# Performance work log

Hardware: AMD Instinct MI355X
Metric: run time of the kernel (lower is better)

## Reference

```python
import jax, jax.numpy as jnp
import numpy as np

L = 12; D = 768; H = 12; HD = D // H
P = 16; IMG = 224; NPATCH = (IMG // P) ** 2
NCLS = 1000; B = 32
GAMMA = 0.01; MIN_TOKENS = 16; EPS = 1e-6
SCALE = HD ** -0.5


def _ln(x, w, b, eps=1e-6):
    mu = x.mean(-1, keepdims=True)
    var = ((x - mu) ** 2).mean(-1, keepdims=True)
    return (x - mu) * jax.lax.rsqrt(var + eps) * w + b


def setup_inputs() -> dict:
    key = jax.random.key(0)
    ks = jax.random.split(key, 16)
    s = 0.02
    rn = lambda k, shape: jax.random.normal(k, shape, jnp.float32) * s
    return {
        'x': jax.random.normal(ks[0], (B, 3, IMG, IMG), jnp.float32),
        'patch_w': rn(ks[1], (D, 3, P, P)),
        'patch_b': jnp.zeros((D,), jnp.float32),
        'cls_token': rn(ks[2], (1, 1, D)),
        'pos_embed': rn(ks[3], (1, NPATCH + 1, D)),
        'ln1_w': jnp.ones((L, D), jnp.float32), 'ln1_b': jnp.zeros((L, D), jnp.float32),
        'qkv_w': rn(ks[4], (L, D, 3 * D)), 'qkv_b': jnp.zeros((L, 3 * D), jnp.float32),
        'proj_w': rn(ks[5], (L, D, D)), 'proj_b': jnp.zeros((L, D), jnp.float32),
        'ln2_w': jnp.ones((L, D), jnp.float32), 'ln2_b': jnp.zeros((L, D), jnp.float32),
        'fc1_w': rn(ks[6], (L, D, 4 * D)), 'fc1_b': jnp.zeros((L, 4 * D), jnp.float32),
        'fc2_w': rn(ks[7], (L, 4 * D, D)), 'fc2_b': jnp.zeros((L, D), jnp.float32),
        'norm_w': jnp.ones((D,), jnp.float32), 'norm_b': jnp.zeros((D,), jnp.float32),
        'head_w': rn(ks[8], (D, NCLS)), 'head_b': jnp.zeros((NCLS,), jnp.float32),
    }


def _block(x, i, ln1_w, ln1_b, qkv_w, qkv_b, proj_w, proj_b, ln2_w, ln2_b, fc1_w, fc1_b, fc2_w, fc2_b):
    Bb, Ntok, _ = x.shape
    xn = _ln(x, ln1_w[i], ln1_b[i])
    qkv = (xn @ qkv_w[i] + qkv_b[i]).reshape(Bb, Ntok, 3, H, HD)
    qkv = qkv.transpose(2, 0, 3, 1, 4)  # [3, B, H, N, hd]
    q, k, v = qkv[0], qkv[1], qkv[2]
    # full N x N attention matrix, materialized as in the original module
    attn = jax.nn.softmax(jnp.einsum('bhqd,bhkd->bhqk', q, k) * SCALE, axis=-1)
    out = jnp.einsum('bhqk,bhkd->bhqd', attn, v)
    out = out.transpose(0, 2, 1, 3).reshape(Bb, Ntok, D) @ proj_w[i] + proj_b[i]
    x = x + out
    h = _ln(x, ln2_w[i], ln2_b[i])
    h = jax.nn.gelu(h @ fc1_w[i] + fc1_b[i], approximate=False)
    x = x + (h @ fc2_w[i] + fc2_b[i])
    return x, attn, v


def _importance(attn, v, eps):
    # Jacobian proxy: d(CLS)/d(patch_j) ~ attn[CLS->j] * ||v_j||
    v_norm = jnp.linalg.norm(v, axis=-1)            # [B, H, N]
    jac = attn[:, :, 0, 1:] * v_norm[:, :, 1:]       # [B, H, Npatch]
    importance = jac.mean(axis=(0, 1))               # batch-shared [Npatch]
    mass = importance.sum()
    rho = importance.std() / (importance.mean() + eps)
    return importance, mass, rho


def _keep_ratio(rho, mass, prev_mass, gamma, eps):
    drift = jnp.abs(mass - prev_mass) / (prev_mass + eps)
    return jnp.clip(1.0 - gamma * rho * (1.0 + drift), 0.0, 1.0)


def _select(importance, n_keep):
    _, idx = jax.lax.top_k(importance, n_keep)
    idx = jnp.sort(idx) + 1  # shift past CLS
    return jnp.concatenate([jnp.zeros((1,), idx.dtype), idx])  # always keep CLS


def reference(x, patch_w, patch_b, cls_token, pos_embed, ln1_w, ln1_b, qkv_w, qkv_b,
              proj_w, proj_b, ln2_w, ln2_b, fc1_w, fc1_b, fc2_w, fc2_b,
              norm_w, norm_b, head_w, head_b):
    Bb = x.shape[0]
    feat = jax.lax.conv_general_dilated(x, patch_w, (P, P), 'VALID',
                                        dimension_numbers=('NCHW', 'OIHW', 'NCHW'))
    feat = feat.reshape(Bb, D, NPATCH).transpose(0, 2, 1) + patch_b  # [B, 196, D]
    xx = jnp.concatenate([jnp.broadcast_to(cls_token, (Bb, 1, D)), feat], axis=1) + pos_embed
    N = NPATCH
    prev_mass = None
    for i in range(L):
        xx, attn, v = _block(xx, i, ln1_w, ln1_b, qkv_w, qkv_b, proj_w, proj_b,
                             ln2_w, ln2_b, fc1_w, fc1_b, fc2_w, fc2_b)
        if N <= MIN_TOKENS:
            prev_mass = None
            continue
        imp, mass, rho = _importance(attn, v, EPS)
        if prev_mass is not None:
            kr = float(_keep_ratio(rho, mass, prev_mass, GAMMA, EPS))
            n_next = max(MIN_TOKENS, int(N * kr))
        else:
            n_next = N
        if n_next < N:
            keep_idx = _select(imp, n_next)
            xx = jnp.take(xx, keep_idx, axis=1)
            N = n_next
        prev_mass = mass
    xx = _ln(xx, norm_w, norm_b)
    return xx[:, 0] @ head_w + head_b
```

## Files before the change

kernel.cpp:

```cpp
#include <hip/hip_runtime.h>
#include <math.h>

#define DEV_INLINE __device__ __forceinline__

constexpr int BB     = 32;
constexpr int DMODEL = 768;
constexpr int NHEAD  = 12;
constexpr int NPATCH = 196;
constexpr int NTOK   = 197;
constexpr int NLAYER = 12;
constexpr int NCLASS = 1000;
constexpr int MTOT   = BB * NTOK;
constexpr int MPAD   = 6400;

typedef __attribute__((ext_vector_type(4))) float f32x4;
typedef __attribute__((ext_vector_type(8))) short bf16x8;

DEV_INLINE void split2(float x, unsigned short& hi, unsigned short& lo) {
    unsigned u = __builtin_bit_cast(unsigned, x);
    unsigned r = (u + 0x7FFFu + ((u >> 16) & 1u)) >> 16;
    hi = (unsigned short)r;
    float fh = __builtin_bit_cast(float, r << 16);
    float l = x - fh;
    unsigned ul = __builtin_bit_cast(unsigned, l);
    lo = (unsigned short)((ul + 0x7FFFu + ((ul >> 16) & 1u)) >> 16);
}

DEV_INLINE unsigned split_pack(float x) {
    unsigned short h, l; split2(x, h, l);
    return (unsigned)h | ((unsigned)l << 16);
}

DEV_INLINE float bf2f(unsigned short s) {
    return __builtin_bit_cast(float, ((unsigned)s) << 16);
}

DEV_INLINE void gload16(const unsigned short* g, unsigned short* l) {
    __builtin_amdgcn_global_load_lds(
        (const __attribute__((address_space(1))) unsigned int*)g,
        (__attribute__((address_space(3))) unsigned int*)l, 16, 0, 0);
}

DEV_INLINE int aswz(int m, int k) {
    return (k & ~31) + ((((k >> 3) & 3) ^ ((m >> 1) & 3)) << 3) + (k & 7);
}

DEV_INLINE float block_reduce_sum(float v, float* sbuf) {
    #pragma unroll
    for (int off = 32; off > 0; off >>= 1) v += __shfl_down(v, off, 64);
    int lane = threadIdx.x & 63, w = threadIdx.x >> 6;
    __syncthreads();
    if (lane == 0) sbuf[w] = v;
    __syncthreads();
    return sbuf[0] + sbuf[1] + sbuf[2] + sbuf[3];
}

__global__ void state_init(int* nTokPtr, int* prevValidPtr) {
    *nTokPtr = NTOK;
    *prevValidPtr = 0;
}

__global__ __launch_bounds__(256)
void cls_init(const float* __restrict__ cls, const float* __restrict__ pos,
              float* __restrict__ tok) {
    int b = blockIdx.x;
    for (int i = threadIdx.x; i < DMODEL; i += 256)
        tok[(size_t)b * NTOK * DMODEL + i] = cls[i] + pos[i];
}

__global__ __launch_bounds__(256)
void wconv_patch(const float* __restrict__ src, unsigned short* __restrict__ hi,
                 unsigned short* __restrict__ lo) {
    int id = blockIdx.x * 256 + threadIdx.x;
    if (id >= 768 * 96) return;
    int n = id / 96, ch = id % 96;
    int k = ch * 8;
    float4 a = *(const float4*)(src + (size_t)n * 768 + k);
    float4 b = *(const float4*)(src + (size_t)n * 768 + k + 4);
    unsigned short h[8], l[8];
    split2(a.x,h[0],l[0]); split2(a.y,h[1],l[1]); split2(a.z,h[2],l[2]); split2(a.w,h[3],l[3]);
    split2(b.x,h[4],l[4]); split2(b.y,h[5],l[5]); split2(b.z,h[6],l[6]); split2(b.w,h[7],l[7]);
    int npanel = n >> 7, c = n & 127;
    int kbi = k >> 5, chunk = (k >> 3) & 3;
    size_t base = ((size_t)npanel * 24 + kbi) * 4096
                + c * 32 + ((chunk ^ ((c >> 1) & 3)) << 3);
    bf16x8 hv, lv;
    #pragma unroll
    for (int j = 0; j < 8; ++j) { hv[j] = (short)h[j]; lv[j] = (short)l[j]; }
    *(bf16x8*)(hi + base) = hv;
    *(bf16x8*)(lo + base) = lv;
}

constexpr size_t WOFF_QKV  = 0;
constexpr size_t WOFF_PROJ = (size_t)768 * 2304;
constexpr size_t WOFF_FC1  = WOFF_PROJ + (size_t)768 * 768;
constexpr size_t WOFF_FC2  = WOFF_FC1 + (size_t)768 * 3072;
constexpr size_t WTOTAL    = WOFF_FC2 + (size_t)3072 * 768;

__global__ __launch_bounds__(256)
void wconv_layer(const float* __restrict__ qkvw, const float* __restrict__ projw,
                 const float* __restrict__ fc1w, const float* __restrict__ fc2w,
                 unsigned short* __restrict__ hi, unsigned short* __restrict__ lo) {
    __shared__ float tile[32][33];
    int bid = blockIdx.x;
    const float* src; int Kd, Nd; size_t dofs;
    if (bid < 1728)      { src = qkvw;  Kd = 768;  Nd = 2304; dofs = WOFF_QKV; }
    else if (bid < 2304) { bid -= 1728; src = projw; Kd = 768;  Nd = 768;  dofs = WOFF_PROJ; }
    else if (bid < 4608) { bid -= 2304; src = fc1w;  Kd = 768;  Nd = 3072; dofs = WOFF_FC1; }
    else                 { bid -= 4608; src = fc2w;  Kd = 3072; Nd = 768;  dofs = WOFF_FC2; }
    const int nkb = Kd >> 5;
    int ntx = Nd / 32;
    int n0 = (bid % ntx) * 32, k0 = (bid / ntx) * 32;
    int tx = threadIdx.x & 31, ty = threadIdx.x >> 5;
    #pragma unroll
    for (int i = 0; i < 32; i += 8)
        tile[ty + i][tx] = src[(size_t)(k0 + ty + i) * Nd + n0 + tx];
    __syncthreads();
    int t = threadIdx.x;
    if (t < 128) {
        int nl = t >> 2, chunk = t & 3;
        unsigned short h[8], l[8];
        #pragma unroll
        for (int j = 0; j < 8; ++j) split2(tile[chunk * 8 + j][nl], h[j], l[j]);
        int n = n0 + nl, k = k0 + chunk * 8;
        int npanel = n >> 7, c = n & 127;
        int kbi = k >> 5;
        size_t base = dofs + ((size_t)npanel * nkb + kbi) * 4096
                    + c * 32 + ((chunk ^ ((c >> 1) & 3)) << 3);
        bf16x8 hv, lv;
        #pragma unroll
        for (int j = 0; j < 8; ++j) { hv[j] = (short)h[j]; lv[j] = (short)l[j]; }
        *(bf16x8*)(hi + base) = hv;
        *(bf16x8*)(lo + base) = lv;
    }
}

template<int ASRC, int EPI>
__global__ __launch_bounds__(256)
void mfma_gemm(const unsigned short* __restrict__ Ahp,
               const unsigned short* __restrict__ Alp,
               const float* __restrict__ Af,
               const unsigned short* __restrict__ Wht,
               const unsigned short* __restrict__ Wlt,
               const float* __restrict__ bias,
               const float* __restrict__ resid,
               void* __restrict__ C, void* __restrict__ C2,
               int ldc, int K, int Mtot, int gm, int gn,
               const int* __restrict__ nTokPtr) {
    const int nTok = (ASRC == 0) ? *nTokPtr : NTOK;
    int nb = gm * gn;
    int o = blockIdx.x;
    int qd = nb >> 3, r8 = nb & 7;
    int xcd = o & 7, wi = o >> 3;
    int fin = (xcd < r8 ? xcd * (qd + 1) : r8 * (qd + 1) + (xcd - r8) * qd) + wi;
    int bm = fin / gn, bn = fin - bm * gn;
    const int m0 = bm * 128, n0 = bn * 128;
    if (m0 >= Mtot) return;
    if (ASRC == 0) {
        int ts = m0 % NTOK;
        if (!(ts < nTok || ts + 128 > NTOK)) return;
    }
    __shared__ unsigned short LDSu[16384];
    unsigned short* AhL = LDSu;
    unsigned short* AlL = LDSu + 4096;
    unsigned short* BhL = LDSu + 8192;
    unsigned short* BlL = LDSu + 12288;
    const int tid = threadIdx.x;
    const int lane = tid & 63, wid = tid >> 6;
    const int wm = wid >> 1, wn = wid & 1;
    const int fr = lane & 15, fg = lane >> 4;

    f32x4 acc[4][4];
    #pragma unroll
    for (int i = 0; i < 4; ++i)
        #pragma unroll
        for (int j = 0; j < 4; ++j) acc[i][j] = (f32x4){0.f, 0.f, 0.f, 0.f};

    const int nkb = K >> 5;
    const int wbase = wid * 512;
    const int g8 = tid * 8;

    int arow = 0, acp = 0, axor = 0, aoff0 = 0, aoff1 = 0;
    bool aval = false; size_t abase = 0;
    if constexpr (ASRC == 1) {
        arow = tid >> 1;
        acp  = (tid & 1) * 2;
        int am = m0 + arow;
        aval = am < Mtot;
        int b = am / NPATCH, pp = am - b * NPATCH;
        int py = pp / 14, px = pp - py * 14;
        abase = (size_t)b * (3 * 224 * 224) + (size_t)(py * 16) * 224 + px * 16;
        axor = (arow >> 1) & 3;
        aoff0 = arow * 32 + ((acp ^ axor) << 3);
        aoff1 = arow * 32 + (((acp + 1) ^ axor) << 3);
    }
    size_t arow_g = 0;
    if constexpr (ASRC == 0)
        arow_g = (size_t)(m0 + (tid >> 2)) * K + (tid & 3) * 8;

    for (int kbi = 0; kbi < nkb; ++kbi) {
        {
            size_t tb = ((size_t)bn * nkb + kbi) * 4096 + g8;
            gload16(Wht + tb,        &BhL[wbase]);
            gload16(Wht + tb + 2048, &BhL[wbase + 2048]);
            gload16(Wlt + tb,        &BlL[wbase]);
            gload16(Wlt + tb + 2048, &BlL[wbase + 2048]);
        }
        if constexpr (ASRC == 0) {
            size_t ab = arow_g + (size_t)kbi * 32;
            gload16(Ahp + ab,                  &AhL[wbase]);
            gload16(Ahp + ab + (size_t)64 * K, &AhL[wbase + 2048]);
            gload16(Alp + ab,                  &AlL[wbase]);
            gload16(Alp + ab + (size_t)64 * K, &AlL[wbase + 2048]);
        } else {
            const int kb = kbi << 5;
            float f[16] = {0,0,0,0,0,0,0,0,0,0,0,0,0,0,0,0};
            if (aval) {
                int k = kb + acp * 8;
                size_t off = abase + (size_t)(k >> 8) * (224 * 224)
                           + (size_t)((k >> 4) & 15) * 224;
                *(float4*)&f[0]  = *(const float4*)(Af + off);
                *(float4*)&f[4]  = *(const float4*)(Af + off + 4);
                *(float4*)&f[8]  = *(const float4*)(Af + off + 8);
                *(float4*)&f[12] = *(const float4*)(Af + off + 12);
            }
            unsigned ph[8], pl[8];
            #pragma unroll
            for (int j = 0; j < 8; ++j) {
                unsigned short h0, l0, h1, l1;
                split2(f[2 * j], h0, l0); split2(f[2 * j + 1], h1, l1);
                ph[j] = (unsigned)h0 | ((unsigned)h1 << 16);
                pl[j] = (unsigned)l0 | ((unsigned)l1 << 16);
            }
            *(uint4*)&AhL[aoff0] = *(uint4*)&ph[0];
            *(uint4*)&AhL[aoff1] = *(uint4*)&ph[4];
            *(uint4*)&AlL[aoff0] = *(uint4*)&pl[0];
            *(uint4*)&AlL[aoff1] = *(uint4*)&pl[4];
        }
        __syncthreads();
        bf16x8 ah[4], al4[4], bh4[4], bl4[4];
        #pragma unroll
        for (int i = 0; i < 4; ++i) {
            int row = wm * 64 + i * 16 + fr;
            int aoff = row * 32 + ((fg ^ ((row >> 1) & 3)) << 3);
            ah[i]  = *(const bf16x8*)&AhL[aoff];
            al4[i] = *(const bf16x8*)&AlL[aoff];
            int col = wn * 64 + i * 16 + fr;
            int boff = col * 32 + ((fg ^ ((col >> 1) & 3)) << 3);
            bh4[i] = *(const bf16x8*)&BhL[boff];
            bl4[i] = *(const bf16x8*)&BlL[boff];
        }
        #pragma unroll
        for (int i = 0; i < 4; ++i)
            #pragma unroll
            for (int j = 0; j < 4; ++j) {
                acc[i][j] = __builtin_amdgcn_mfma_f32_16x16x32_bf16(ah[i],  bh4[j], acc[i][j], 0, 0, 0);
                acc[i][j] = __builtin_amdgcn_mfma_f32_16x16x32_bf16(ah[i],  bl4[j], acc[i][j], 0, 0, 0);
                acc[i][j] = __builtin_amdgcn_mfma_f32_16x16x32_bf16(al4[i], bh4[j], acc[i][j], 0, 0, 0);
            }
        __syncthreads();
    }
    if constexpr (EPI == 0 || EPI == 2) {
        unsigned pk[4][4][4];
        #pragma unroll
        for (int i = 0; i < 4; ++i)
            #pragma unroll
            for (int j = 0; j < 4; ++j)
                #pragma unroll
                for (int e = 0; e < 4; ++e) {
                    int n = n0 + wn * 64 + j * 16 + fr;
                    float v = acc[i][j][e] + bias[n];
                    if constexpr (EPI == 2)
                        v = 0.5f * v * (1.0f + erff(v * 0.70710678118654752f));
                    pk[i][j][e] = split_pack(v);
                }
        const int rr = tid >> 4, cc = tid & 15;
        #pragma unroll
        for (int plane = 0; plane < 2; ++plane) {
            __syncthreads();
            #pragma unroll
            for (int i = 0; i < 4; ++i)
                #pragma unroll
                for (int j = 0; j < 4; ++j)
                    #pragma unroll
                    for (int e = 0; e < 4; ++e) {
                        int r = wm * 64 + i * 16 + fg * 4 + e;
                        int c = wn * 64 + j * 16 + fr;
                        LDSu[r * 128 + c] = (unsigned short)
                            (plane ? (pk[i][j][e] >> 16) : (pk[i][j][e] & 0xffffu));
                    }
            __syncthreads();
            unsigned short* Cp = (unsigned short*)(plane ? C2 : C);
            #pragma unroll
            for (int p = 0; p < 8; ++p) {
                int r = p * 16 + rr;
                int m = m0 + r;
                if (m < Mtot && (m % NTOK) < nTok) {
                    size_t dst;
                    if constexpr (EPI == 0)
                        dst = (size_t)m * ldc + n0 + cc * 8;
                    else
                        dst = (size_t)m * ldc + n0 + (cc >> 2) * 32
                            + (((cc & 3) ^ ((m >> 1) & 3)) << 3);
                    *(bf16x8*)(Cp + dst) = *(const bf16x8*)&LDSu[r * 128 + cc * 8];
                }
            }
        }
    } else {
        #pragma unroll
        for (int i = 0; i < 4; ++i)
            #pragma unroll
            for (int j = 0; j < 4; ++j)
                #pragma unroll
                for (int e = 0; e < 4; ++e) {
                    int m = m0 + wm * 64 + i * 16 + fg * 4 + e;
                    int n = n0 + wn * 64 + j * 16 + fr;
                    if (m >= Mtot) continue;
                    if (ASRC == 0 && (m % NTOK) >= nTok) continue;
                    float v = acc[i][j][e] + bias[n];
                    if constexpr (EPI == 1) {
                        ((float*)C)[(size_t)m * ldc + n] = v + resid[(size_t)m * ldc + n];
                    } else {
                        int b = m / NPATCH, pp = m - b * NPATCH;
                        v += resid[(size_t)(1 + pp) * DMODEL + n];
                        ((float*)C)[((size_t)b * NTOK + 1 + pp) * DMODEL + n] = v;
                    }
                }
    }
}

__global__ __launch_bounds__(256)
void ln_tok(const float* __restrict__ X, unsigned short* __restrict__ Yh,
            unsigned short* __restrict__ Yl,
            const float* __restrict__ w, const float* __restrict__ b,
            const int* __restrict__ nTokPtr) {
    int m = blockIdx.x;
    if ((m % NTOK) >= *nTokPtr) return;
    __shared__ float sbuf[4];
    __shared__ float yb[768];
    const float* x = X + (size_t)m * DMODEL;
    int tid = threadIdx.x;
    float v[3];
    #pragma unroll
    for (int i = 0; i < 3; i++) v[i] = x[tid + i * 256];
    float mu = block_reduce_sum(v[0] + v[1] + v[2], sbuf) * (1.0f / 768.0f);
    float d2 = 0.f;
    #pragma unroll
    for (int i = 0; i < 3; i++) { float d = v[i] - mu; d2 = fmaf(d, d, d2); }
    float var = block_reduce_sum(d2, sbuf) * (1.0f / 768.0f);
    float rstd = rsqrtf(var + 1e-6f);
    #pragma unroll
    for (int i = 0; i < 3; i++) {
        int idx = tid + i * 256;
        yb[idx] = (v[i] - mu) * rstd * w[idx] + b[idx];
    }
    __syncthreads();
    if (tid < 96) {
        bf16x8 hv, lv;
        #pragma unroll
        for (int j = 0; j < 8; ++j) {
            unsigned short h, l; split2(yb[tid * 8 + j], h, l);
            hv[j] = (short)h; lv[j] = (short)l;
        }
        size_t dst = (size_t)m * 768 + (tid >> 2) * 32
                   + (((tid & 3) ^ ((m >> 1) & 3)) << 3);
        *(bf16x8*)(Yh + dst) = hv;
        *(bf16x8*)(Yl + dst) = lv;
    }
}

__global__ __launch_bounds__(256)
void ln_cls(const float* __restrict__ X, float* __restrict__ Y,
            const float* __restrict__ w, const float* __restrict__ b) {
    int bb = blockIdx.x;
    __shared__ float sbuf[4];
    const float* x = X + (size_t)bb * NTOK * DMODEL;
    int tid = threadIdx.x;
    float v[3];
    #pragma unroll
    for (int i = 0; i < 3; i++) v[i] = x[tid + i * 256];
    float mu = block_reduce_sum(v[0] + v[1] + v[2], sbuf) * (1.0f / 768.0f);
    float d2 = 0.f;
    #pragma unroll
    for (int i = 0; i < 3; i++) { float d = v[i] - mu; d2 = fmaf(d, d, d2); }
    float var = block_reduce_sum(d2, sbuf) * (1.0f / 768.0f);
    float rstd = rsqrtf(var + 1e-6f);
    #pragma unroll
    for (int i = 0; i < 3; i++) {
        int idx = tid + i * 256;
        Y[(size_t)bb * DMODEL + idx] = (v[i] - mu) * rstd * w[idx] + b[idx];
    }
}

__global__ __launch_bounds__(256)
void attn_v4(const unsigned short* __restrict__ qh_g,
             const unsigned short* __restrict__ ql_g,
             unsigned short* __restrict__ oh_g,
             unsigned short* __restrict__ ol_g,
             float* __restrict__ jacg, const int* __restrict__ nTokPtr) {
    const int nTok = *nTokPtr;
    const int bh = blockIdx.x;
    const int b = bh / NHEAD, h = bh % NHEAD;
    const int q0 = blockIdx.y * 32;
    if (q0 >= nTok) return;
    __shared__ unsigned short Kh[64 * 64], Kl[64 * 64];
    __shared__ unsigned short Vth[64 * 64], Vtl[64 * 64];
    __shared__ unsigned short Ph[32 * 64], Pl[32 * 64];
    __shared__ float Ss[32][68];
    __shared__ float mrow[32], lrow[32], frow[32];
    __shared__ float s0row[256], vnrow[256];
    __shared__ float vnpart[64][4];
    const int tid = threadIdx.x;
    const int lane = tid & 63, wv = tid >> 6;
    const int fr = lane & 15, fg = lane >> 4;
    const int qh = wv >> 1, xh = wv & 1;

    bf16x8 qah[2], qal[2];
    {
        int q = q0 + qh * 16 + fr;
        int qe = q < nTok ? q : nTok - 1;
        const unsigned short* qrh = qh_g + (size_t)(b * NTOK + qe) * 2304 + h * 64;
        const unsigned short* qrl = ql_g + (size_t)(b * NTOK + qe) * 2304 + h * 64;
        #pragma unroll
        for (int s = 0; s < 2; ++s) {
            qah[s] = *(const bf16x8*)(qrh + s * 32 + fg * 8);
            qal[s] = *(const bf16x8*)(qrl + s * 32 + fg * 8);
        }
    }
    if (tid < 32) { mrow[tid] = -INFINITY; lrow[tid] = 0.f; frow[tid] = 1.f; }
    f32x4 oacc[2] = {{0,0,0,0},{0,0,0,0}};
    const int njt = (nTok + 63) >> 6;
    const int sj = tid & 63, sdh = tid >> 6;

    for (int jt = 0; jt < njt; ++jt) {
        const int jb = jt * 64;
        __syncthreads();
        {
            int j = jb + sj;
            bf16x8 kh0, kh1, kl0, kl1, vh0, vh1, vl0, vl1;
            if (j < nTok) {
                size_t rp = (size_t)(b * NTOK + j) * 2304 + h * 64;
                kh0 = *(const bf16x8*)(qh_g + rp + 768 + sdh * 16);
                kh1 = *(const bf16x8*)(qh_g + rp + 768 + sdh * 16 + 8);
                kl0 = *(const bf16x8*)(ql_g + rp + 768 + sdh * 16);
                kl1 = *(const bf16x8*)(ql_g + rp + 768 + sdh * 16 + 8);
                vh0 = *(const bf16x8*)(qh_g + rp + 1536 + sdh * 16);
                vh1 = *(const bf16x8*)(qh_g + rp + 1536 + sdh * 16 + 8);
                vl0 = *(const bf16x8*)(ql_g + rp + 1536 + sdh * 16);
                vl1 = *(const bf16x8*)(ql_g + rp + 1536 + sdh * 16 + 8);
            } else {
                bf16x8 z = {0,0,0,0,0,0,0,0};
                kh0=kh1=kl0=kl1=vh0=vh1=vl0=vl1 = z;
            }
            int c0 = sdh * 2;
            int ko0 = sj * 64 + ((c0 ^ (sj & 7)) << 3);
            int ko1 = sj * 64 + (((c0 + 1) ^ (sj & 7)) << 3);
            *(bf16x8*)&Kh[ko0] = kh0; *(bf16x8*)&Kh[ko1] = kh1;
            *(bf16x8*)&Kl[ko0] = kl0; *(bf16x8*)&Kl[ko1] = kl1;
            float pn = 0.f;
            #pragma unroll
            for (int i = 0; i < 16; ++i) {
                unsigned short vh = (unsigned short)(i < 8 ? vh0[i] : vh1[i - 8]);
                unsigned short vl = (unsigned short)(i < 8 ? vl0[i] : vl1[i - 8]);
                int d = sdh * 16 + i;
                int si = d * 64 + (((sj >> 3) ^ (d & 7)) << 3) + (sj & 7);
                Vth[si] = vh; Vtl[si] = vl;
                if (q0 == 0) {
                    float vf = bf2f(vh) + bf2f(vl);
                    pn = fmaf(vf, vf, pn);
                }
            }
            if (q0 == 0) vnpart[sj][sdh] = pn;
        }
        __syncthreads();
        {
            f32x4 sacc[2] = {{0,0,0,0},{0,0,0,0}};
            #pragma unroll
            for (int s = 0; s < 2; ++s)
                #pragma unroll
                for (int t = 0; t < 2; ++t) {
                    int j = xh * 32 + t * 16 + fr;
                    int off = j * 64 + (((s * 4 + fg) ^ (j & 7)) << 3);
                    bf16x8 kbh = *(const bf16x8*)&Kh[off];
                    bf16x8 kbl = *(const bf16x8*)&Kl[off];
                    sacc[t] = __builtin_amdgcn_mfma_f32_16x16x32_bf16(qah[s], kbh, sacc[t], 0, 0, 0);
                    sacc[t] = __builtin_amdgcn_mfma_f32_16x16x32_bf16(qah[s], kbl, sacc[t], 0, 0, 0);
                    sacc[t] = __builtin_amdgcn_mfma_f32_16x16x32_bf16(qal[s], kbh, sacc[t], 0, 0, 0);
                }
            #pragma unroll
            for (int t = 0; t < 2; ++t)
                #pragma unroll
                for (int e = 0; e < 4; ++e) {
                    int q = q0 + qh * 16 + fg * 4 + e;
                    int j = jb + xh * 32 + t * 16 + fr;
                    Ss[qh * 16 + fg * 4 + e][xh * 32 + t * 16 + fr] =
                        (q < nTok && j < nTok) ? sacc[t][e] * 0.125f : -INFINITY;
                }
        }
        __syncthreads();
        {
            int q = tid >> 3, s = tid & 7;
            bool rowok = (q0 + q) < nTok;
            float4 va = *(const float4*)&Ss[q][s * 8];
            float4 vb = *(const float4*)&Ss[q][s * 8 + 4];
            if (q0 == 0 && q == 0) {
                *(float4*)&s0row[jb + s * 8] = va;
                *(float4*)&s0row[jb + s * 8 + 4] = vb;
            }
            float mx = fmaxf(fmaxf(fmaxf(va.x, va.y), fmaxf(va.z, va.w)),
                             fmaxf(fmaxf(vb.x, vb.y), fmaxf(vb.z, vb.w)));
            #pragma unroll
            for (int o = 1; o < 8; o <<= 1) mx = fmaxf(mx, __shfl_xor(mx, o));
            float mold = mrow[q];
            float mnew = fmaxf(mold, mx);
            float e[8];
            float sum = 0.f;
            if (rowok) {
                e[0] = expf(va.x - mnew); e[1] = expf(va.y - mnew);
                e[2] = expf(va.z - mnew); e[3] = expf(va.w - mnew);
                e[4] = expf(vb.x - mnew); e[5] = expf(vb.y - mnew);
                e[6] = expf(vb.z - mnew); e[7] = expf(vb.w - mnew);
                sum = ((e[0] + e[1]) + (e[2] + e[3])) + ((e[4] + e[5]) + (e[6] + e[7]));
            } else {
                #pragma unroll
                for (int i = 0; i < 8; ++i) e[i] = 0.f;
            }
            #pragma unroll
            for (int o = 1; o < 8; o <<= 1) sum += __shfl_xor(sum, o);
            bf16x8 ph, pl;
            #pragma unroll
            for (int i = 0; i < 8; ++i) {
                unsigned u = __builtin_bit_cast(unsigned, e[i]);
                ph[i] = (short)(u >> 16);
                float r = e[i] - __builtin_bit_cast(float, u & 0xffff0000u);
                pl[i] = (short)(__builtin_bit_cast(unsigned, r) >> 16);
            }
            int poff = q * 64 + ((s ^ (q & 7)) << 3);
            *(bf16x8*)&Ph[poff] = ph;
            *(bf16x8*)&Pl[poff] = pl;
            if (s == 0 && rowok) {
                float f = expf(mold - mnew);
                lrow[q] = lrow[q] * f + sum;
                mrow[q] = mnew;
                frow[q] = f;
            }
            if (q0 == 0 && tid < 64) {
                int jj = jb + tid;
                if (jj < nTok)
                    vnrow[jj] = sqrtf(vnpart[tid][0] + vnpart[tid][1]
                                    + vnpart[tid][2] + vnpart[tid][3]);
            }
        }
        __syncthreads();
        {
            float fe[4];
            #pragma unroll
            for (int e = 0; e < 4; ++e) fe[e] = frow[qh * 16 + fg * 4 + e];
            #pragma unroll
            for (int t = 0; t < 2; ++t)
                #pragma unroll
                for (int e = 0; e < 4; ++e) oacc[t][e] *= fe[e];
            #pragma unroll
            for (int s = 0; s < 2; ++s) {
                int pr = qh * 16 + fr;
                int poff = pr * 64 + (((s * 4 + fg) ^ (pr & 7)) << 3);
                bf16x8 pah = *(const bf16x8*)&Ph[poff];
                bf16x8 pal = *(const bf16x8*)&Pl[poff];
                #pragma unroll
                for (int t = 0; t < 2; ++t) {
                    int d = xh * 32 + t * 16 + fr;
                    int voff = d * 64 + (((s * 4 + fg) ^ (d & 7)) << 3);
                    bf16x8 vbh = *(const bf16x8*)&Vth[voff];
                    bf16x8 vbl = *(const bf16x8*)&Vtl[voff];
                    oacc[t] = __builtin_amdgcn_mfma_f32_16x16x32_bf16(pah, vbh, oacc[t], 0, 0, 0);
                    oacc[t] = __builtin_amdgcn_mfma_f32_16x16x32_bf16(pah, vbl, oacc[t], 0, 0, 0);
                    oacc[t] = __builtin_amdgcn_mfma_f32_16x16x32_bf16(pal, vbh, oacc[t], 0, 0, 0);
                }
            }
        }
    }
    #pragma unroll
    for (int e = 0; e < 4; ++e) {
        int qr = qh * 16 + fg * 4 + e;
        int q = q0 + qr;
        if (q < nTok) {
            float inv = 1.0f / lrow[qr];
            int m = b * NTOK + q;
            int xr = (m >> 1) & 3;
            #pragma unroll
            for (int t = 0; t < 2; ++t) {
                int n = h * 64 + xh * 32 + t * 16 + fr;
                unsigned short hh, ll;
                split2(oacc[t][e] * inv, hh, ll);
                size_t dst = (size_t)m * 768 + (n & ~31)
                           + ((((n >> 3) & 3) ^ xr) << 3) + (n & 7);
                oh_g[dst] = hh; ol_g[dst] = ll;
            }
        }
    }
    if (q0 == 0) {
        float m0f = mrow[0], l0 = lrow[0];
        for (int j = 1 + tid; j < nTok; j += 256)
            jacg[(size_t)bh * NPATCH + (j - 1)] = (expf(s0row[j] - m0f) / l0) * vnrow[j];
    }
}

__global__ __launch_bounds__(256)
void decide_kernel(const float* __restrict__ jac,
                   int* __restrict__ nTokPtr, int* __restrict__ nTokNextPtr,
                   int* __restrict__ keepIdx, float* __restrict__ prevMassPtr,
                   int* __restrict__ prevValidPtr) {
    const int nTok = *nTokPtr;
    const int N = nTok - 1;
    const int tid = threadIdx.x;
    if (N <= 16) {
        if (tid == 0) { *prevValidPtr = 0; *nTokNextPtr = nTok; }
        for (int t = tid; t < nTok; t += 256) keepIdx[t] = t;
        return;
    }
    __shared__ float impF[NPATCH];
    __shared__ int   sel[NPATCH];
    __shared__ int   s_next;
    for (int j = tid; j < N; j += 256) {
        double s = 0.0;
        for (int r = 0; r < BB * NHEAD; r++) s += (double)jac[(size_t)r * NPATCH + j];
        impF[j] = (float)(s * (1.0 / 384.0));
    }
    __syncthreads();
    if (tid == 0) {
        double ms = 0.0;
        for (int j = 0; j < N; j++) ms += (double)impF[j];
        float massF = (float)ms;
        float meanF = (float)(ms / (double)N);
        double vs = 0.0;
        for (int j = 0; j < N; j++) { double d = (double)impF[j] - (double)meanF; vs += d * d; }
        float stdF = (float)sqrt(vs / (double)N);
        float rho = stdF / (meanF + 1e-6f);
        int nnext;
        if (*prevValidPtr != 0) {
            float pm = *prevMassPtr;
            float drift = fabsf(massF - pm) / (pm + 1e-6f);
            float kr = 1.0f - 0.01f * rho * (1.0f + drift);
            kr = fminf(fmaxf(kr, 0.0f), 1.0f);
            int t = (int)((double)N * (double)kr);
            nnext = t < 16 ? 16 : t;
        } else {
            nnext = N;
        }
        *prevMassPtr = massF;
        *prevValidPtr = 1;
        s_next = nnext;
        *nTokNextPtr = nnext + 1;
    }
    __syncthreads();
    int nnext = s_next;
    if (nnext < N) {
        for (int j = tid; j < N; j += 256) {
            float vj = impF[j];
            int rank = 0;
            for (int i = 0; i < N; i++) {
                float vi = impF[i];
                rank += (vi > vj || (vi == vj && i < j)) ? 1 : 0;
            }
            sel[j] = (rank < nnext) ? 1 : 0;
        }
        __syncthreads();
        if (tid == 0) {
            int c = 1;
            keepIdx[0] = 0;
            for (int j = 0; j < N; j++) if (sel[j]) keepIdx[c++] = j + 1;
        }
    } else {
        for (int t = tid; t < nTok; t += 256) keepIdx[t] = t;
    }
}

__global__ __launch_bounds__(192)
void gather_kernel(const float* __restrict__ src, float* __restrict__ dst,
                   const int* __restrict__ keepIdx,
                   const int* __restrict__ nTokNextPtr, int* __restrict__ nTokPtr) {
    int nn = *nTokNextPtr;
    int m = blockIdx.x;
    int b = m / NTOK, t = m - b * NTOK;
    if (t < nn) {
        int s = keepIdx[t];
        const float4* sp = (const float4*)(src + ((size_t)b * NTOK + s) * DMODEL);
        float4* dp = (float4*)(dst + ((size_t)b * NTOK + t) * DMODEL);
        dp[threadIdx.x] = sp[threadIdx.x];
    }
    if (m == 0 && threadIdx.x == 0) *nTokPtr = nn;
}

__global__ __launch_bounds__(256)
void head_kernel(const float* __restrict__ lnC, const float* __restrict__ W,
                 const float* __restrict__ hb, float* __restrict__ out) {
    int b = blockIdx.x;
    int n = blockIdx.y * 256 + threadIdx.x;
    __shared__ float xs[DMODEL];
    for (int i = threadIdx.x; i < DMODEL; i += 256) xs[i] = lnC[(size_t)b * DMODEL + i];
    __syncthreads();
    if (n < NCLASS) {
        float acc = hb[n];
        for (int d = 0; d < DMODEL; d++) acc = fmaf(xs[d], W[(size_t)d * NCLASS + n], acc);
        out[(size_t)b * NCLASS + n] = acc;
    }
}

extern "C" void kernel_launch(void* const* d_in, const int* in_sizes, int n_in,
                              void* d_out, int out_size, void* d_ws, size_t ws_size,
                              hipStream_t stream) {
    const float* x       = (const float*)d_in[0];
    const float* patch_w = (const float*)d_in[1];
    const float* patch_b = (const float*)d_in[2];
    const float* cls_tok = (const float*)d_in[3];
    const float* pos     = (const float*)d_in[4];
    const float* ln1_w   = (const float*)d_in[5];
    const float* ln1_b   = (const float*)d_in[6];
    const float* qkv_w   = (const float*)d_in[7];
    const float* qkv_b   = (const float*)d_in[8];
    const float* proj_w  = (const float*)d_in[9];
    const float* proj_b  = (const float*)d_in[10];
    const float* ln2_w   = (const float*)d_in[11];
    const float* ln2_b   = (const float*)d_in[12];
    const float* fc1_w   = (const float*)d_in[13];
    const float* fc1_b   = (const float*)d_in[14];
    const float* fc2_w   = (const float*)d_in[15];
    const float* fc2_b   = (const float*)d_in[16];
    const float* norm_w  = (const float*)d_in[17];
    const float* norm_b  = (const float*)d_in[18];
    const float* head_w  = (const float*)d_in[19];
    const float* head_b  = (const float*)d_in[20];
    float* out = (float*)d_out;

    char* ws = (char*)d_ws;
    size_t off = 0;
    auto alloc = [&](size_t nbytes) {
        char* p = ws + off;
        off += ((nbytes + 255) / 256) * 256;
        return p;
    };
    float* tokA = (float*)alloc((size_t)MTOT * DMODEL * 4);
    float* tokB = (float*)alloc((size_t)MTOT * DMODEL * 4);
    char* uni = alloc((size_t)2 * MPAD * 3072 * 2);
    unsigned short* qkvh = (unsigned short*)uni;
    unsigned short* qkvl = qkvh + (size_t)MTOT * 2304;
    unsigned short* hbh  = (unsigned short*)uni;
    unsigned short* hbl  = hbh + (size_t)MPAD * 3072;
    unsigned short* xnh  = (unsigned short*)alloc((size_t)MPAD * DMODEL * 2);
    unsigned short* xnl  = (unsigned short*)alloc((size_t)MPAD * DMODEL * 2);
    unsigned short* outh = (unsigned short*)alloc((size_t)MPAD * DMODEL * 2);
    unsigned short* outl = (unsigned short*)alloc((size_t)MPAD * DMODEL * 2);
    unsigned short* whi  = (unsigned short*)alloc(WTOTAL * 2);
    unsigned short* wlo  = (unsigned short*)alloc(WTOTAL * 2);
    unsigned short* wphi = (unsigned short*)alloc((size_t)768 * 768 * 2);
    unsigned short* wplo = (unsigned short*)alloc((size_t)768 * 768 * 2);
    float* jac  = (float*)alloc((size_t)BB * NHEAD * NPATCH * 4);
    float* lnC  = (float*)alloc((size_t)BB * DMODEL * 4);
    float* prevMass = (float*)alloc(32);
    int* ints = (int*)alloc(1024);
    int* nTokP = ints; int* nTokNextP = ints + 1; int* prevValidP = ints + 2;
    int* keepIdx = ints + 4;

    dim3 blk(256);
    state_init<<<dim3(1), dim3(1), 0, stream>>>(nTokP, prevValidP);
    wconv_patch<<<dim3(288), blk, 0, stream>>>(patch_w, wphi, wplo);
    cls_init<<<dim3(BB), blk, 0, stream>>>(cls_tok, pos, tokA);
    mfma_gemm<1, 3><<<dim3(49 * 6), blk, 0, stream>>>(
        nullptr, nullptr, x, wphi, wplo, patch_b, pos, tokA, nullptr,
        DMODEL, 768, BB * NPATCH, 49, 6, nTokP);

    float* bufs[2] = {tokA, tokB};
    const int gm = MPAD / 128;
    for (int l = 0; l < NLAYER; l++) {
        float* cur = bufs[l & 1];
        float* nxt = bufs[(l + 1) & 1];
        wconv_layer<<<dim3(6912), blk, 0, stream>>>(
            qkv_w + (size_t)l * 768 * 2304, proj_w + (size_t)l * 768 * 768,
            fc1_w + (size_t)l * 768 * 3072, fc2_w + (size_t)l * 3072 * 768, whi, wlo);
        ln_tok<<<dim3(MTOT), blk, 0, stream>>>(cur, xnh, xnl,
            ln1_w + l * 768, ln1_b + l * 768, nTokP);
        mfma_gemm<0, 0><<<dim3(gm * 18), blk, 0, stream>>>(
            xnh, xnl, nullptr, whi + WOFF_QKV, wlo + WOFF_QKV, qkv_b + (size_t)l * 2304,
            nullptr, qkvh, qkvl, 2304, 768, MTOT, gm, 18, nTokP);
        attn_v4<<<dim3(BB * NHEAD, 7), blk, 0, stream>>>(qkvh, qkvl, outh, outl, jac, nTokP);
        mfma_gemm<0, 1><<<dim3(gm * 6), blk, 0, stream>>>(
            outh, outl, nullptr, whi + WOFF_PROJ, wlo + WOFF_PROJ, proj_b + (size_t)l * 768,
            cur, cur, nullptr, 768, 768, MTOT, gm, 6, nTokP);
        ln_tok<<<dim3(MTOT), blk, 0, stream>>>(cur, xnh, xnl,
            ln2_w + l * 768, ln2_b + l * 768, nTokP);
        mfma_gemm<0, 2><<<dim3(gm * 24), blk, 0, stream>>>(
            xnh, xnl, nullptr, whi + WOFF_FC1, wlo + WOFF_FC1, fc1_b + (size_t)l * 3072,
            nullptr, hbh, hbl, 3072, 768, MTOT, gm, 24, nTokP);
        mfma_gemm<0, 1><<<dim3(gm * 6), blk, 0, stream>>>(
            hbh, hbl, nullptr, whi + WOFF_FC2, wlo + WOFF_FC2, fc2_b + (size_t)l * 768,
            cur, cur, nullptr, 768, 3072, MTOT, gm, 6, nTokP);
        decide_kernel<<<dim3(1), blk, 0, stream>>>(jac, nTokP, nTokNextP, keepIdx,
                                                   prevMass, prevValidP);
        gather_kernel<<<dim3(MTOT), dim3(192), 0, stream>>>(cur, nxt, keepIdx, nTokNextP, nTokP);
    }
    ln_cls<<<dim3(BB), blk, 0, stream>>>(bufs[0], lnC, norm_w, norm_b);
    head_kernel<<<dim3(BB, 4), blk, 0, stream>>>(lnC, head_w, head_b, out);
}
```

Baseline: 7.198 ms.

## Double-buffer GEMM LDS tiles and simplify bf16 split epilogue to direct stores

Converts the split-bf16 GEMM main loop to double-buffered LDS, issuing next k-block global->LDS loads (and the im2col register prefetch for the patch GEMM) before the MFMA work on the current buffer, with one barrier per iteration. The epilogue that staged bf16 hi/lo planes through LDS for vectorized 16-byte stores is replaced by direct scalar 2-byte stores from accumulators. This aims to hide global load latency behind MFMA, but doubles LDS use (64KB), which may reduce occupancy, and the scalar epilogue stores are less coalesced. The qkvl offset is also moved to MPAD stride.

```diff
diff --git a/kernel.cpp b/kernel.cpp
--- a/kernel.cpp
+++ b/kernel.cpp
@@ -26,11 +26,6 @@
     lo = (unsigned short)((ul + 0x7FFFu + ((ul >> 16) & 1u)) >> 16);
 }
 
-DEV_INLINE unsigned split_pack(float x) {
-    unsigned short h, l; split2(x, h, l);
-    return (unsigned)h | ((unsigned)l << 16);
-}
-
 DEV_INLINE float bf2f(unsigned short s) {
     return __builtin_bit_cast(float, ((unsigned)s) << 16);
 }
@@ -39,10 +34,6 @@
     __builtin_amdgcn_global_load_lds(
         (const __attribute__((address_space(1))) unsigned int*)g,
         (__attribute__((address_space(3))) unsigned int*)l, 16, 0, 0);
-}
-
-DEV_INLINE int aswz(int m, int k) {
-    return (k & ~31) + ((((k >> 3) & 3) ^ ((m >> 1) & 3)) << 3) + (k & 7);
 }
 
 DEV_INLINE float block_reduce_sum(float v, float* sbuf) {
@@ -160,11 +151,8 @@
         int ts = m0 % NTOK;
         if (!(ts < nTok || ts + 128 > NTOK)) return;
     }
-    __shared__ unsigned short LDSu[16384];
-    unsigned short* AhL = LDSu;
-    unsigned short* AlL = LDSu + 4096;
-    unsigned short* BhL = LDSu + 8192;
-    unsigned short* BlL = LDSu + 12288;
+    __shared__ unsigned short Ah[2][4096], Al[2][4096];
+    __shared__ unsigned short Bh[2][4096], Bl[2][4096];
     const int tid = threadIdx.x;
     const int lane = tid & 63, wid = tid >> 6;
     const int wm = wid >> 1, wn = wid & 1;
@@ -180,7 +168,11 @@
     const int wbase = wid * 512;
     const int g8 = tid * 8;
 
-    int arow = 0, acp = 0, axor = 0, aoff0 = 0, aoff1 = 0;
+    size_t arow_g = 0;
+    if constexpr (ASRC == 0)
+        arow_g = (size_t)(m0 + (tid >> 2)) * K + (tid & 3) * 8;
+
+    int arow = 0, acp = 0, aoff0 = 0, aoff1 = 0;
     bool aval = false; size_t abase = 0;
     if constexpr (ASRC == 1) {
         arow = tid >> 1;
@@ -190,66 +182,80 @@
         int b = am / NPATCH, pp = am - b * NPATCH;
         int py = pp / 14, px = pp - py * 14;
         abase = (size_t)b * (3 * 224 * 224) + (size_t)(py * 16) * 224 + px * 16;
-        axor = (arow >> 1) & 3;
+        int axor = (arow >> 1) & 3;
         aoff0 = arow * 32 + ((acp ^ axor) << 3);
         aoff1 = arow * 32 + (((acp + 1) ^ axor) << 3);
     }
-    size_t arow_g = 0;
-    if constexpr (ASRC == 0)
-        arow_g = (size_t)(m0 + (tid >> 2)) * K + (tid & 3) * 8;
-
-    for (int kbi = 0; kbi < nkb; ++kbi) {
-        {
-            size_t tb = ((size_t)bn * nkb + kbi) * 4096 + g8;
-            gload16(Wht + tb,        &BhL[wbase]);
-            gload16(Wht + tb + 2048, &BhL[wbase + 2048]);
-            gload16(Wlt + tb,        &BlL[wbase]);
-            gload16(Wlt + tb + 2048, &BlL[wbase + 2048]);
-        }
+
+    float4 freg[4];
+    auto issueA = [&](int kbi, int bufSel) {
         if constexpr (ASRC == 0) {
-            size_t ab = arow_g + (size_t)kbi * 32;
-            gload16(Ahp + ab,                  &AhL[wbase]);
-            gload16(Ahp + ab + (size_t)64 * K, &AhL[wbase + 2048]);
-            gload16(Alp + ab,                  &AlL[wbase]);
-            gload16(Alp + ab + (size_t)64 * K, &AlL[wbase + 2048]);
+            size_t ab = arow_g + (size_t)(kbi << 5);
+            gload16(Ahp + ab,                  &Ah[bufSel][wbase]);
+            gload16(Ahp + ab + (size_t)64 * K, &Ah[bufSel][wbase + 2048]);
+            gload16(Alp + ab,                  &Al[bufSel][wbase]);
+            gload16(Alp + ab + (size_t)64 * K, &Al[bufSel][wbase + 2048]);
         } else {
-            const int kb = kbi << 5;
-            float f[16] = {0,0,0,0,0,0,0,0,0,0,0,0,0,0,0,0};
             if (aval) {
-                int k = kb + acp * 8;
+                int k = (kbi << 5) + acp * 8;
                 size_t off = abase + (size_t)(k >> 8) * (224 * 224)
                            + (size_t)((k >> 4) & 15) * 224;
-                *(float4*)&f[0]  = *(const float4*)(Af + off);
-                *(float4*)&f[4]  = *(const float4*)(Af + off + 4);
-                *(float4*)&f[8]  = *(const float4*)(Af + off + 8);
-                *(float4*)&f[12] = *(const float4*)(Af + off + 12);
-            }
-            unsigned ph[8], pl[8];
-            #pragma unroll
-            for (int j = 0; j < 8; ++j) {
-                unsigned short h0, l0, h1, l1;
-                split2(f[2 * j], h0, l0); split2(f[2 * j + 1], h1, l1);
-                ph[j] = (unsigned)h0 | ((unsigned)h1 << 16);
-                pl[j] = (unsigned)l0 | ((unsigned)l1 << 16);
-            }
-            *(uint4*)&AhL[aoff0] = *(uint4*)&ph[0];
-            *(uint4*)&AhL[aoff1] = *(uint4*)&ph[4];
-            *(uint4*)&AlL[aoff0] = *(uint4*)&pl[0];
-            *(uint4*)&AlL[aoff1] = *(uint4*)&pl[4];
-        }
-        __syncthreads();
+                freg[0] = *(const float4*)(Af + off);
+                freg[1] = *(const float4*)(Af + off + 4);
+                freg[2] = *(const float4*)(Af + off + 8);
+                freg[3] = *(const float4*)(Af + off + 12);
+            } else {
+                freg[0] = freg[1] = freg[2] = freg[3] = make_float4(0.f, 0.f, 0.f, 0.f);
+            }
+        }
+    };
+    auto storeA = [&](int bufSel) {
+        unsigned ph[8], pl[8];
+        const float* f = (const float*)&freg[0];
+        #pragma unroll
+        for (int j = 0; j < 8; ++j) {
+            unsigned short h0, l0, h1, l1;
+            split2(f[2 * j], h0, l0); split2(f[2 * j + 1], h1, l1);
+            ph[j] = (unsigned)h0 | ((unsigned)h1 << 16);
+            pl[j] = (unsigned)l0 | ((unsigned)l1 << 16);
+        }
+        *(uint4*)&Ah[bufSel][aoff0] = *(uint4*)&ph[0];
+        *(uint4*)&Ah[bufSel][aoff1] = *(uint4*)&ph[4];
+        *(uint4*)&Al[bufSel][aoff0] = *(uint4*)&pl[0];
+        *(uint4*)&Al[bufSel][aoff1] = *(uint4*)&pl[4];
+    };
+    auto issueB = [&](int kbi, int bufSel) {
+        size_t tb = ((size_t)bn * nkb + kbi) * 4096 + g8;
+        gload16(Wht + tb,        &Bh[bufSel][wbase]);
+        gload16(Wht + tb + 2048, &Bh[bufSel][wbase + 2048]);
+        gload16(Wlt + tb,        &Bl[bufSel][wbase]);
+        gload16(Wlt + tb + 2048, &Bl[bufSel][wbase + 2048]);
+    };
+
+    issueB(0, 0);
+    issueA(0, 0);
+    if constexpr (ASRC == 1) storeA(0);
+    __syncthreads();
+
+    for (int kbi = 0; kbi < nkb; ++kbi) {
+        const int cur = kbi & 1;
         bf16x8 ah[4], al4[4], bh4[4], bl4[4];
         #pragma unroll
         for (int i = 0; i < 4; ++i) {
             int row = wm * 64 + i * 16 + fr;
             int aoff = row * 32 + ((fg ^ ((row >> 1) & 3)) << 3);
-            ah[i]  = *(const bf16x8*)&AhL[aoff];
-            al4[i] = *(const bf16x8*)&AlL[aoff];
+            ah[i]  = *(const bf16x8*)&Ah[cur][aoff];
+            al4[i] = *(const bf16x8*)&Al[cur][aoff];
             int col = wn * 64 + i * 16 + fr;
             int boff = col * 32 + ((fg ^ ((col >> 1) & 3)) << 3);
-            bh4[i] = *(const bf16x8*)&BhL[boff];
-            bl4[i] = *(const bf16x8*)&BlL[boff];
-        }
+            bh4[i] = *(const bf16x8*)&Bh[cur][boff];
+            bl4[i] = *(const bf16x8*)&Bl[cur][boff];
+        }
+        if (kbi + 1 < nkb) {
+            issueB(kbi + 1, cur ^ 1);
+            issueA(kbi + 1, cur ^ 1);
+        }
+        __builtin_amdgcn_sched_barrier(0);
         #pragma unroll
         for (int i = 0; i < 4; ++i)
             #pragma unroll
@@ -258,74 +264,44 @@
                 acc[i][j] = __builtin_amdgcn_mfma_f32_16x16x32_bf16(ah[i],  bl4[j], acc[i][j], 0, 0, 0);
                 acc[i][j] = __builtin_amdgcn_mfma_f32_16x16x32_bf16(al4[i], bh4[j], acc[i][j], 0, 0, 0);
             }
-        __syncthreads();
-    }
-    if constexpr (EPI == 0 || EPI == 2) {
-        unsigned pk[4][4][4];
-        #pragma unroll
-        for (int i = 0; i < 4; ++i)
-            #pragma unroll
-            for (int j = 0; j < 4; ++j)
-                #pragma unroll
-                for (int e = 0; e < 4; ++e) {
-                    int n = n0 + wn * 64 + j * 16 + fr;
-                    float v = acc[i][j][e] + bias[n];
+        __builtin_amdgcn_sched_barrier(0);
+        if (kbi + 1 < nkb) {
+            if constexpr (ASRC == 1) storeA(cur ^ 1);
+            __syncthreads();
+        }
+    }
+    #pragma unroll
+    for (int i = 0; i < 4; ++i) {
+        #pragma unroll
+        for (int j = 0; j < 4; ++j) {
+            #pragma unroll
+            for (int e = 0; e < 4; ++e) {
+                int m = m0 + wm * 64 + i * 16 + fg * 4 + e;
+                int n = n0 + wn * 64 + j * 16 + fr;
+                if (m >= Mtot) continue;
+                if (ASRC == 0 && (m % NTOK) >= nTok) continue;
+                float v = acc[i][j][e] + bias[n];
+                if constexpr (EPI == 0 || EPI == 2) {
                     if constexpr (EPI == 2)
                         v = 0.5f * v * (1.0f + erff(v * 0.70710678118654752f));
-                    pk[i][j][e] = split_pack(v);
-                }
-        const int rr = tid >> 4, cc = tid & 15;
-        #pragma unroll
-        for (int plane = 0; plane < 2; ++plane) {
-            __syncthreads();
-            #pragma unroll
-            for (int i = 0; i < 4; ++i)
-                #pragma unroll
-                for (int j = 0; j < 4; ++j)
-                    #pragma unroll
-                    for (int e = 0; e < 4; ++e) {
-                        int r = wm * 64 + i * 16 + fg * 4 + e;
-                        int c = wn * 64 + j * 16 + fr;
-                        LDSu[r * 128 + c] = (unsigned short)
-                            (plane ? (pk[i][j][e] >> 16) : (pk[i][j][e] & 0xffffu));
-                    }
-            __syncthreads();
-            unsigned short* Cp = (unsigned short*)(plane ? C2 : C);
-            #pragma unroll
-            for (int p = 0; p < 8; ++p) {
-                int r = p * 16 + rr;
-                int m = m0 + r;
-                if (m < Mtot && (m % NTOK) < nTok) {
+                    unsigned short h, l; split2(v, h, l);
                     size_t dst;
                     if constexpr (EPI == 0)
-                        dst = (size_t)m * ldc + n0 + cc * 8;
+                        dst = (size_t)m * ldc + n;
                     else
-                        dst = (size_t)m * ldc + n0 + (cc >> 2) * 32
-                            + (((cc & 3) ^ ((m >> 1) & 3)) << 3);
-                    *(bf16x8*)(Cp + dst) = *(const bf16x8*)&LDSu[r * 128 + cc * 8];
+                        dst = (size_t)m * ldc + (n & ~31)
+                            + ((((n >> 3) & 3) ^ ((m >> 1) & 3)) << 3) + (n & 7);
+                    ((unsigned short*)C)[dst]  = h;
+                    ((unsigned short*)C2)[dst] = l;
+                } else if constexpr (EPI == 1) {
+                    ((float*)C)[(size_t)m * ldc + n] = v + resid[(size_t)m * ldc + n];
+                } else {
+                    int b = m / NPATCH, pp = m - b * NPATCH;
+                    v += resid[(size_t)(1 + pp) * DMODEL + n];
+                    ((float*)C)[((size_t)b * NTOK + 1 + pp) * DMODEL + n] = v;
                 }
             }
         }
-    } else {
-        #pragma unroll
-        for (int i = 0; i < 4; ++i)
-            #pragma unroll
-            for (int j = 0; j < 4; ++j)
-                #pragma unroll
-                for (int e = 0; e < 4; ++e) {
-                    int m = m0 + wm * 64 + i * 16 + fg * 4 + e;
-                    int n = n0 + wn * 64 + j * 16 + fr;
-                    if (m >= Mtot) continue;
-                    if (ASRC == 0 && (m % NTOK) >= nTok) continue;
-                    float v = acc[i][j][e] + bias[n];
-                    if constexpr (EPI == 1) {
-                        ((float*)C)[(size_t)m * ldc + n] = v + resid[(size_t)m * ldc + n];
-                    } else {
-                        int b = m / NPATCH, pp = m - b * NPATCH;
-                        v += resid[(size_t)(1 + pp) * DMODEL + n];
-                        ((float*)C)[((size_t)b * NTOK + 1 + pp) * DMODEL + n] = v;
-                    }
-                }
     }
 }
 
@@ -743,7 +719,7 @@
     float* tokB = (float*)alloc((size_t)MTOT * DMODEL * 4);
     char* uni = alloc((size_t)2 * MPAD * 3072 * 2);
     unsigned short* qkvh = (unsigned short*)uni;
-    unsigned short* qkvl = qkvh + (size_t)MTOT * 2304;
+    unsigned short* qkvl = qkvh + (size_t)MPAD * 2304;
     unsigned short* hbh  = (unsigned short*)uni;
     unsigned short* hbl  = hbh + (size_t)MPAD * 3072;
     unsigned short* xnh  = (unsigned short*)alloc((size_t)MPAD * DMODEL * 2);
```

New measurement: 5.946 ms (median of 2 runs). -17.4%, faster.
